# Kernel tuning notes

Hardware: AMD Instinct MI355X
Metric: run time of the kernel (lower is better)

The kernel has to match this reference:

```python
import jax, jax.numpy as jnp
import numpy as np

B, S, D, F, E = 4, 1024, 768, 3072, 8
TOP_K = 2


def setup_inputs() -> dict:
    key = jax.random.key(0)
    k0, k1, k2, k3 = jax.random.split(key, 4)
    x = jax.random.normal(k0, (B, S, D), dtype=jnp.float32)
    w_router = jax.random.normal(k1, (D, E), dtype=jnp.float32) * 0.02
    w1 = jax.random.normal(k2, (E, D, F), dtype=jnp.float32) * 0.02
    b1 = jnp.zeros((E, F), dtype=jnp.float32)
    w2 = jax.random.normal(k3, (E, F, D), dtype=jnp.float32) * 0.02
    b2 = jnp.zeros((E, D), dtype=jnp.float32)
    return {"x": x, "w_router": w_router, "w1": w1, "b1": b1, "w2": w2, "b2": b2}


def reference(x, w_router, w1, b1, w2, b2):
    # Router: logits [B,S,E] -> softmax -> top-k -> renormalize
    router_logits = jnp.einsum('bsd,de->bse', x, w_router)
    router_probs = jax.nn.softmax(router_logits, axis=-1)
    top_k_probs, top_k_idx = jax.lax.top_k(router_probs, TOP_K)  # [B,S,K]
    top_k_probs = top_k_probs / (jnp.sum(top_k_probs, axis=-1, keepdims=True) + 1e-8)
    # Combine weights [B,S,E]: weight for expert e if selected, else 0.
    # (top-k indices are distinct, so summing one-hots over k is exact.)
    combine = jnp.sum(
        jax.nn.one_hot(top_k_idx, E, dtype=x.dtype) * top_k_probs[..., None], axis=-2)
    # Dense per-expert FFN over ALL tokens (faithful to the original masked-dense math).
    h = jax.nn.gelu(jnp.einsum('bsd,edf->ebsf', x, w1) + b1[:, None, None, :],
                    approximate=False)  # [E,B,S,F]
    expert_out = jnp.einsum('ebsf,efd->ebsd', h, w2) + b2[:, None, None, :]  # [E,B,S,D]
    output = jnp.einsum('ebsd,bse->bsd', expert_out, combine)
    return output
```

## Files before the change

kernel.cpp:

```cpp
#include <hip/hip_runtime.h>
#include <math.h>

typedef __bf16 bf16x8 __attribute__((ext_vector_type(8)));
typedef float f32x4 __attribute__((ext_vector_type(4)));

#define B_ 4
#define S_ 1024
#define D_ 768
#define F_ 3072
#define E_ 8
#define NTOK 4096
#define NSLOTP 9216

__device__ __forceinline__ void gload_lds16(const void* g, void* s) {
  __builtin_amdgcn_global_load_lds((const __attribute__((address_space(1))) void*)g,
                                   (__attribute__((address_space(3))) void*)s, 16, 0, 0);
}

__device__ __forceinline__ float gelu_f(float v) {
  float u = v * (0.7978845608f + 0.0356774081f * v * v);
  float t = 1.f - 2.f / (1.f + __expf(2.f * u));
  return 0.5f * v * (1.f + t);
}

__global__ __launch_bounds__(256) void k_router(const float* __restrict__ x,
    const float* __restrict__ wr, int* __restrict__ tki, float* __restrict__ tkw) {
  int wid = threadIdx.x >> 6, lane = threadIdx.x & 63;
  int t = blockIdx.x * 4 + wid;
  const float* xp = x + (size_t)t * D_;
  float pa[E_];
#pragma unroll
  for (int e = 0; e < E_; ++e) pa[e] = 0.f;
#pragma unroll
  for (int it = 0; it < D_ / 64; ++it) {
    int d = it * 64 + lane;
    float xv = xp[d];
    const float4* wp = (const float4*)(wr + (size_t)d * E_);
    float4 a = wp[0], b = wp[1];
    pa[0] += xv * a.x; pa[1] += xv * a.y; pa[2] += xv * a.z; pa[3] += xv * a.w;
    pa[4] += xv * b.x; pa[5] += xv * b.y; pa[6] += xv * b.z; pa[7] += xv * b.w;
  }
#pragma unroll
  for (int e = 0; e < E_; ++e) {
    float v = pa[e];
    for (int off = 32; off; off >>= 1) v += __shfl_xor(v, off);
    pa[e] = v;
  }
  if (lane == 0) {
    float m = pa[0];
#pragma unroll
    for (int e = 1; e < E_; ++e) m = fmaxf(m, pa[e]);
    float p[E_], s = 0.f;
#pragma unroll
    for (int e = 0; e < E_; ++e) { p[e] = expf(pa[e] - m); s += p[e]; }
#pragma unroll
    for (int e = 0; e < E_; ++e) p[e] = p[e] / s;
    int i0 = 0; float b0 = p[0];
#pragma unroll
    for (int e = 1; e < E_; ++e) if (p[e] > b0) { b0 = p[e]; i0 = e; }
    int i1 = -1; float b1v = -1.f;
#pragma unroll
    for (int e = 0; e < E_; ++e) if (e != i0 && p[e] > b1v) { b1v = p[e]; i1 = e; }
    float den = b0 + b1v + 1e-8f;
    tki[t * 2] = i0; tki[t * 2 + 1] = i1;
    tkw[t * 2] = b0 / den; tkw[t * 2 + 1] = b1v / den;
  }
}

__global__ __launch_bounds__(256) void k_route_all(const int* __restrict__ tki,
    int* __restrict__ stok, int* __restrict__ tslot, int* __restrict__ aoff) {
  __shared__ int cl[256][E_];
  __shared__ int tot[E_];
  __shared__ int aoffA[E_ + 1];
  int tid = threadIdx.x;
  for (int i = tid; i < NSLOTP; i += 256) stok[i] = -1;
#pragma unroll
  for (int e = 0; e < E_; ++e) cl[tid][e] = 0;
  int t0 = tid * (NTOK / 256);
#pragma unroll
  for (int i = 0; i < NTOK / 256; ++i) {
    cl[tid][tki[(t0 + i) * 2]]++;
    cl[tid][tki[(t0 + i) * 2 + 1]]++;
  }
  __syncthreads();
  if (tid < E_) {
    int run = 0;
    for (int i = 0; i < 256; ++i) { int v = cl[i][tid]; cl[i][tid] = run; run += v; }
    tot[tid] = run;
  }
  __syncthreads();
  if (tid == 0) {
    int a = 0; aoffA[0] = 0; aoff[0] = 0;
    for (int e = 0; e < E_; ++e) { a += ((tot[e] + 127) >> 7) << 7; aoffA[e + 1] = a; aoff[e + 1] = a; }
  }
  __syncthreads();
#pragma unroll
  for (int i = 0; i < NTOK / 256; ++i) {
    int t = t0 + i;
#pragma unroll
    for (int k = 0; k < 2; ++k) {
      int e = tki[t * 2 + k];
      int pos = aoffA[e] + cl[tid][e];
      cl[tid][e]++;
      stok[pos] = t;
      tslot[t * 2 + k] = pos;
    }
  }
}

__global__ __launch_bounds__(256) void k_gather(const float* __restrict__ x,
    const int* __restrict__ stok, __bf16* __restrict__ Xg) {
  int i8 = blockIdx.x * 256 + threadIdx.x;
  int flat = i8 * 8;
  int row = flat / D_;
  int col = flat - row * D_;
  int tok = stok[row];
  bf16x8 v;
  if (tok >= 0) {
    const float4* s = (const float4*)(x + (size_t)tok * D_ + col);
    float4 a = s[0], b = s[1];
    v[0] = (__bf16)a.x; v[1] = (__bf16)a.y; v[2] = (__bf16)a.z; v[3] = (__bf16)a.w;
    v[4] = (__bf16)b.x; v[5] = (__bf16)b.y; v[6] = (__bf16)b.z; v[7] = (__bf16)b.w;
  } else {
#pragma unroll
    for (int k = 0; k < 8; ++k) v[k] = (__bf16)0.f;
  }
  *(bf16x8*)(Xg + (size_t)flat) = v;
}

__global__ __launch_bounds__(256) void k_transpose(const float* __restrict__ in,
    __bf16* __restrict__ outp, int R, int C) {
  __shared__ float Ts[64][65];
  int e = blockIdx.z;
  int r0 = blockIdx.y * 64, c0 = blockIdx.x * 64;
  const float* ip = in + (size_t)e * R * C;
  int lr = threadIdx.x >> 4;
  int lc = (threadIdx.x & 15) * 4;
#pragma unroll
  for (int it = 0; it < 4; ++it) {
    int r = lr + it * 16;
    float4 v = *(const float4*)(ip + (size_t)(r0 + r) * C + c0 + lc);
    Ts[r][lc] = v.x; Ts[r][lc + 1] = v.y; Ts[r][lc + 2] = v.z; Ts[r][lc + 3] = v.w;
  }
  __syncthreads();
  int rr = (threadIdx.x & 7) * 8;
  int cc = threadIdx.x >> 3;
  __bf16* op = outp + (size_t)e * R * C + r0 + rr;
#pragma unroll
  for (int it = 0; it < 2; ++it) {
    int c = cc + it * 32;
    bf16x8 v;
#pragma unroll
    for (int i = 0; i < 8; ++i) v[i] = (__bf16)Ts[rr + i][c];
    *(bf16x8*)(op + (size_t)(c0 + c) * R) = v;
  }
}

template<int KST, int N, int MODE, int KSPLIT>
__global__ __launch_bounds__(512, 4) void k_gemm(
    const __bf16* __restrict__ A, const __bf16* __restrict__ Bt,
    const float* __restrict__ bias, const int* __restrict__ aoff,
    __bf16* __restrict__ Hout, float* __restrict__ E0, float* __restrict__ E1) {
  constexpr int BN = 256;
  constexpr int ASZ = 128 * 32;
  constexpr int BSZ = BN * 32;
  constexpr int NK = KST / 32 / KSPLIT;
  constexpr int NB = N / BN;
  constexpr int NMB = NSLOTP / 128;
  constexpr int NWGB = NB * NMB;
  constexpr int NWG = NWGB * KSPLIT;

  __shared__ __align__(16) __bf16 Als[2 * ASZ];
  __shared__ __align__(16) __bf16 Bls[2 * BSZ];

  int bswz = (blockIdx.x & 7) * (NWG / 8) + (blockIdx.x >> 3);
  int kh = bswz / NWGB;
  int rem = bswz % NWGB;
  int mb = rem % NMB, nb = rem / NMB;
  int row0 = mb * 128;
  if (row0 >= aoff[E_]) return;
  int e = 0;
#pragma unroll
  for (int q = 0; q < E_; ++q) if (row0 >= aoff[q + 1]) e = q + 1;
  const __bf16* Bp = Bt + (size_t)e * D_ * F_;
  int kbase = kh * (KST / KSPLIT);

  int tid = threadIdx.x, w = tid >> 6, l = tid & 63;
  int lr = l >> 2, ls = l & 3;
  int fr = l & 15, fg = l >> 4;
  int wrow = (w >> 2) * 64, wcol = (w & 3) * 64;

  auto STAGE = [&](int kt, int b) {
    int k0 = kbase + kt * 32;
    {
      int rowA = w * 16 + lr;
      int sA = ls ^ ((rowA >> 1) & 3);
      gload_lds16(A + (size_t)(row0 + rowA) * KST + k0 + sA * 8, Als + b * ASZ + w * 512);
    }
#pragma unroll
    for (int q = 0; q < 2; ++q) {
      int idx = w * 2 + q;
      int rowB = idx * 16 + lr;
      int sB = ls ^ ((rowB >> 1) & 3);
      gload_lds16(Bp + (size_t)(nb * BN + rowB) * KST + k0 + sB * 8, Bls + b * BSZ + idx * 512);
    }
  };

  f32x4 acc[4][4] = {};
  STAGE(0, 0);
  asm volatile("s_waitcnt vmcnt(0)" ::: "memory");
  __builtin_amdgcn_sched_barrier(0);
  __builtin_amdgcn_s_barrier();
  for (int t = 0; t < NK; ++t) {
    int cur = t & 1;
    if (t + 1 < NK) STAGE(t + 1, cur ^ 1);
    __builtin_amdgcn_sched_barrier(0);
    bf16x8 af[4], bfr[4];
#pragma unroll
    for (int i = 0; i < 4; ++i) {
      int rl = wrow + i * 16 + fr;
      af[i] = *(const bf16x8*)(Als + cur * ASZ + rl * 32 + ((fg ^ ((rl >> 1) & 3)) << 3));
    }
#pragma unroll
    for (int j = 0; j < 4; ++j) {
      int nl = wcol + j * 16 + fr;
      bfr[j] = *(const bf16x8*)(Bls + cur * BSZ + nl * 32 + ((fg ^ ((nl >> 1) & 3)) << 3));
    }
#pragma unroll
    for (int i = 0; i < 4; ++i)
#pragma unroll
      for (int j = 0; j < 4; ++j)
        acc[i][j] = __builtin_amdgcn_mfma_f32_16x16x32_bf16(af[i], bfr[j], acc[i][j], 0, 0, 0);
    __builtin_amdgcn_sched_barrier(0);
    asm volatile("s_waitcnt vmcnt(0)" ::: "memory");
    __builtin_amdgcn_s_barrier();
  }

  if constexpr (MODE == 0) {
#pragma unroll
    for (int j = 0; j < 4; ++j) {
      int col = nb * BN + wcol + j * 16 + fr;
      float bv = bias[e * N + col];
#pragma unroll
      for (int i = 0; i < 4; ++i) {
#pragma unroll
        for (int r = 0; r < 4; ++r) {
          int row = row0 + wrow + i * 16 + fg * 4 + r;
          Hout[(size_t)row * N + col] = (__bf16)gelu_f(acc[i][j][r] + bv);
        }
      }
    }
  } else {
    float* Ep = (kh == 0) ? E0 : E1;
#pragma unroll
    for (int j = 0; j < 4; ++j) {
      int col = nb * BN + wcol + j * 16 + fr;
      float bv = (kh == 0) ? bias[e * N + col] : 0.f;
#pragma unroll
      for (int i = 0; i < 4; ++i) {
#pragma unroll
        for (int r = 0; r < 4; ++r) {
          int row = row0 + wrow + i * 16 + fg * 4 + r;
          Ep[(size_t)row * N + col] = acc[i][j][r] + bv;
        }
      }
    }
  }
}

__global__ __launch_bounds__(256) void k_combine(const float* __restrict__ E0,
    const float* __restrict__ E1, const int* __restrict__ tslot,
    const float* __restrict__ tkw, float* __restrict__ out) {
  int idx = blockIdx.x * 256 + threadIdx.x;
  int t = idx / (D_ / 4);
  int c4 = (idx - t * (D_ / 4)) * 4;
  int s0 = tslot[2 * t], s1 = tslot[2 * t + 1];
  float w0 = tkw[2 * t], w1 = tkw[2 * t + 1];
  float4 a = *(const float4*)(E0 + (size_t)s0 * D_ + c4);
  float4 b = *(const float4*)(E0 + (size_t)s1 * D_ + c4);
  float4 o;
  if (E1) {
    float4 a1 = *(const float4*)(E1 + (size_t)s0 * D_ + c4);
    float4 b1 = *(const float4*)(E1 + (size_t)s1 * D_ + c4);
    o.x = w0 * (a.x + a1.x) + w1 * (b.x + b1.x);
    o.y = w0 * (a.y + a1.y) + w1 * (b.y + b1.y);
    o.z = w0 * (a.z + a1.z) + w1 * (b.z + b1.z);
    o.w = w0 * (a.w + a1.w) + w1 * (b.w + b1.w);
  } else {
    o.x = w0 * a.x + w1 * b.x; o.y = w0 * a.y + w1 * b.y;
    o.z = w0 * a.z + w1 * b.z; o.w = w0 * a.w + w1 * b.w;
  }
  *(float4*)(out + (size_t)t * D_ + c4) = o;
}

extern "C" void kernel_launch(void* const* d_in, const int* in_sizes, int n_in,
                              void* d_out, int out_size, void* d_ws, size_t ws_size,
                              hipStream_t stream) {
  const float* x  = (const float*)d_in[0];
  const float* wr = (const float*)d_in[1];
  const float* w1 = (const float*)d_in[2];
  const float* b1 = (const float*)d_in[3];
  const float* w2 = (const float*)d_in[4];
  const float* b2 = (const float*)d_in[5];
  float* out = (float*)d_out;

  char* ws = (char*)d_ws;
  size_t o = 0;
  __bf16* w1t = (__bf16*)(ws + o); o += (size_t)E_ * D_ * F_ * 2;
  __bf16* Xg  = (__bf16*)(ws + o); o += (size_t)NSLOTP * D_ * 2;
  __bf16* w2t = (__bf16*)(ws + o); o += (size_t)E_ * D_ * F_ * 2;
  __bf16* H   = (__bf16*)(ws + o); o += (size_t)NSLOTP * F_ * 2;
  int*   tki  = (int*)(ws + o);   o += (size_t)NTOK * 2 * 4;
  float* tkw  = (float*)(ws + o); o += (size_t)NTOK * 2 * 4;
  int*   stok = (int*)(ws + o);   o += (size_t)NSLOTP * 4;
  int*   tslot= (int*)(ws + o);   o += (size_t)NTOK * 2 * 4;
  int*   aoff = (int*)(ws + o);   o += 64;
  float* E0   = (float*)w1t;
  float* E1   = (float*)(ws + o);
  size_t oE1  = o + (size_t)NSLOTP * D_ * 4;
  if (ws_size < o) return;
  bool split = (ws_size >= oE1);

  k_router<<<NTOK / 4, 256, 0, stream>>>(x, wr, tki, tkw);
  k_route_all<<<1, 256, 0, stream>>>(tki, stok, tslot, aoff);
  k_gather<<<(NSLOTP * D_ / 8) / 256, 256, 0, stream>>>(x, stok, Xg);
  k_transpose<<<dim3(F_ / 64, D_ / 64, E_), 256, 0, stream>>>(w1, w1t, D_, F_);
  k_transpose<<<dim3(D_ / 64, F_ / 64, E_), 256, 0, stream>>>(w2, w2t, F_, D_);
  k_gemm<D_, F_, 0, 1><<<(F_ / 256) * (NSLOTP / 128), 512, 0, stream>>>(
      Xg, w1t, b1, aoff, H, nullptr, nullptr);
  if (split) {
    k_gemm<F_, D_, 1, 2><<<2 * (D_ / 256) * (NSLOTP / 128), 512, 0, stream>>>(
        H, w2t, b2, aoff, nullptr, E0, E1);
    k_combine<<<NTOK * (D_ / 4) / 256, 256, 0, stream>>>(E0, E1, tslot, tkw, out);
  } else {
    k_gemm<F_, D_, 1, 1><<<(D_ / 256) * (NSLOTP / 128), 512, 0, stream>>>(
        H, w2t, b2, aoff, nullptr, E0, nullptr);
    k_combine<<<NTOK * (D_ / 4) / 256, 256, 0, stream>>>(E0, nullptr, tslot, tkw, out);
  }
}
```

Baseline: 212.9 us.

## Give first expert GEMM a dedicated triple-buffered K=64 pipeline with split MFMA phases

Splits the generic GEMM template into a specialised up-projection kernel and the existing down-projection kernel. The new up-projection kernel uses 64-wide K tiles with three LDS buffers, prefetching two stages ahead. Each iteration is split into two MFMA halves, with the next tile's global-to-LDS loads interleaved between them, explicit vmcnt/lgkmcnt waits, and raised wave priority around the MFMAs. This is meant to hide load latency and reduce barriers per FLOP, at the cost of much larger LDS use that drops occupancy to one workgroup per CU.

```diff
diff --git a/kernel.cpp b/kernel.cpp
--- a/kernel.cpp
+++ b/kernel.cpp
@@ -16,6 +16,15 @@
   __builtin_amdgcn_global_load_lds((const __attribute__((address_space(1))) void*)g,
                                    (__attribute__((address_space(3))) void*)s, 16, 0, 0);
 }
+
+template<int N> __device__ __forceinline__ void wait_vmcnt() {
+  if constexpr (N == 0)      asm volatile("s_waitcnt vmcnt(0)" ::: "memory");
+  else if constexpr (N == 6) asm volatile("s_waitcnt vmcnt(6)" ::: "memory");
+  else static_assert(N == 0, "unhandled vmcnt");
+}
+#define BAR()    asm volatile("s_barrier" ::: "memory")
+#define LGKM0()  do { asm volatile("s_waitcnt lgkmcnt(0)" ::: "memory"); \
+                      __builtin_amdgcn_sched_barrier(0); } while (0)
 
 __device__ __forceinline__ float gelu_f(float v) {
   float u = v * (0.7978845608f + 0.0356774081f * v * v);
@@ -156,11 +165,140 @@
   }
 }
 
-template<int KST, int N, int MODE, int KSPLIT>
-__global__ __launch_bounds__(512, 4) void k_gemm(
+__global__ __launch_bounds__(512, 1) void k_gemm1(
     const __bf16* __restrict__ A, const __bf16* __restrict__ Bt,
     const float* __restrict__ bias, const int* __restrict__ aoff,
-    __bf16* __restrict__ Hout, float* __restrict__ E0, float* __restrict__ E1) {
+    __bf16* __restrict__ Hout) {
+  constexpr int KST = D_;
+  constexpr int N = F_;
+  constexpr int NK = KST / 64;
+  constexpr int ASZ = 128 * 64;
+  constexpr int BSZ = 256 * 64;
+  constexpr int NB = N / 256, NMB = NSLOTP / 128, NWG = NB * NMB;
+
+  __shared__ __align__(16) __bf16 Als[3 * ASZ];
+  __shared__ __align__(16) __bf16 Bls[3 * BSZ];
+
+  int bswz = (blockIdx.x & 7) * (NWG / 8) + (blockIdx.x >> 3);
+  int mb = bswz % NMB, nb = bswz / NMB;
+  int row0 = mb * 128;
+  if (row0 >= aoff[E_]) return;
+  int e = 0;
+#pragma unroll
+  for (int q = 0; q < E_; ++q) if (row0 >= aoff[q + 1]) e = q + 1;
+  const __bf16* Bp = Bt + (size_t)e * D_ * F_;
+
+  int tid = threadIdx.x, w = tid >> 6, l = tid & 63;
+  int fr = l & 15, fg = l >> 4;
+  int wr = w >> 2, wc = w & 3;
+
+  int ur = tid >> 3;
+  int us = tid & 7;
+  int ukk = us >> 2, uf4 = us & 3;
+
+  auto SA = [&](int kt, int b) {
+#pragma unroll
+    for (int u = 0; u < 2; ++u) {
+      int r = u * 64 + ur;
+      int f4s = uf4 ^ ((r >> 1) & 3);
+      gload_lds16(A + (size_t)(row0 + r) * KST + kt * 64 + ukk * 32 + f4s * 8,
+                  Als + b * ASZ + u * 4096 + w * 512);
+    }
+  };
+  auto SB = [&](int kt, int b, int u0, int u1) {
+    for (int u = u0; u < u1; ++u) {
+      int r = u * 64 + ur;
+      int f4s = uf4 ^ ((r >> 1) & 3);
+      gload_lds16(Bp + (size_t)(nb * 256 + r) * KST + kt * 64 + ukk * 32 + f4s * 8,
+                  Bls + b * BSZ + u * 4096 + w * 512);
+    }
+  };
+
+  SA(0, 0); SB(0, 0, 0, 4);
+  SA(1, 1); SB(1, 1, 0, 4);
+
+  f32x4 acc[4][4] = {};
+  for (int t = 0; t < NK; ++t) {
+    int b = t % 3, bs = (t + 2) % 3;
+    bool st = (t + 2) < NK;
+    if (t + 1 < NK) wait_vmcnt<6>(); else wait_vmcnt<0>();
+    BAR();
+    __builtin_amdgcn_sched_barrier(0);
+    const __bf16* Ab = Als + b * ASZ;
+    const __bf16* Bb = Bls + b * BSZ;
+    bf16x8 af[4][2], bf0[2][2];
+#pragma unroll
+    for (int i = 0; i < 4; ++i) {
+      int r = wr * 64 + i * 16 + fr;
+      int sw = ((r >> 1) & 3);
+#pragma unroll
+      for (int kk = 0; kk < 2; ++kk)
+        af[i][kk] = *(const bf16x8*)(Ab + r * 64 + kk * 32 + ((fg ^ sw) << 3));
+    }
+#pragma unroll
+    for (int j = 0; j < 2; ++j) {
+      int n = wc * 64 + j * 16 + fr;
+      int sw = ((n >> 1) & 3);
+#pragma unroll
+      for (int kk = 0; kk < 2; ++kk)
+        bf0[j][kk] = *(const bf16x8*)(Bb + n * 64 + kk * 32 + ((fg ^ sw) << 3));
+    }
+    if (st) { SA(t + 2, bs); SB(t + 2, bs, 0, 2); }
+    LGKM0();
+    __builtin_amdgcn_s_setprio(1);
+#pragma unroll
+    for (int i = 0; i < 4; ++i)
+#pragma unroll
+      for (int j = 0; j < 2; ++j)
+#pragma unroll
+        for (int kk = 0; kk < 2; ++kk)
+          acc[i][j] = __builtin_amdgcn_mfma_f32_16x16x32_bf16(af[i][kk], bf0[j][kk], acc[i][j], 0, 0, 0);
+    __builtin_amdgcn_s_setprio(0);
+    __builtin_amdgcn_sched_barrier(0);
+    BAR();
+    bf16x8 bf1[2][2];
+#pragma unroll
+    for (int j = 0; j < 2; ++j) {
+      int n = wc * 64 + (2 + j) * 16 + fr;
+      int sw = ((n >> 1) & 3);
+#pragma unroll
+      for (int kk = 0; kk < 2; ++kk)
+        bf1[j][kk] = *(const bf16x8*)(Bb + n * 64 + kk * 32 + ((fg ^ sw) << 3));
+    }
+    if (st) SB(t + 2, bs, 2, 4);
+    LGKM0();
+    __builtin_amdgcn_s_setprio(1);
+#pragma unroll
+    for (int i = 0; i < 4; ++i)
+#pragma unroll
+      for (int j = 0; j < 2; ++j)
+#pragma unroll
+        for (int kk = 0; kk < 2; ++kk)
+          acc[i][2 + j] = __builtin_amdgcn_mfma_f32_16x16x32_bf16(af[i][kk], bf1[j][kk], acc[i][2 + j], 0, 0, 0);
+    __builtin_amdgcn_s_setprio(0);
+    __builtin_amdgcn_sched_barrier(0);
+  }
+
+#pragma unroll
+  for (int j = 0; j < 4; ++j) {
+    int col = nb * 256 + wc * 64 + j * 16 + fr;
+    float bv = bias[e * N + col];
+#pragma unroll
+    for (int i = 0; i < 4; ++i) {
+#pragma unroll
+      for (int r = 0; r < 4; ++r) {
+        int row = row0 + wr * 64 + i * 16 + fg * 4 + r;
+        Hout[(size_t)row * N + col] = (__bf16)gelu_f(acc[i][j][r] + bv);
+      }
+    }
+  }
+}
+
+template<int KST, int N, int KSPLIT>
+__global__ __launch_bounds__(512, 4) void k_gemm2(
+    const __bf16* __restrict__ A, const __bf16* __restrict__ Bt,
+    const float* __restrict__ bias, const int* __restrict__ aoff,
+    float* __restrict__ E0, float* __restrict__ E1) {
   constexpr int BN = 256;
   constexpr int ASZ = 128 * 32;
   constexpr int BSZ = BN * 32;
@@ -236,33 +374,17 @@
     __builtin_amdgcn_s_barrier();
   }
 
-  if constexpr (MODE == 0) {
-#pragma unroll
-    for (int j = 0; j < 4; ++j) {
-      int col = nb * BN + wcol + j * 16 + fr;
-      float bv = bias[e * N + col];
-#pragma unroll
-      for (int i = 0; i < 4; ++i) {
-#pragma unroll
-        for (int r = 0; r < 4; ++r) {
-          int row = row0 + wrow + i * 16 + fg * 4 + r;
-          Hout[(size_t)row * N + col] = (__bf16)gelu_f(acc[i][j][r] + bv);
-        }
-      }
-    }
-  } else {
-    float* Ep = (kh == 0) ? E0 : E1;
-#pragma unroll
-    for (int j = 0; j < 4; ++j) {
-      int col = nb * BN + wcol + j * 16 + fr;
-      float bv = (kh == 0) ? bias[e * N + col] : 0.f;
-#pragma unroll
-      for (int i = 0; i < 4; ++i) {
-#pragma unroll
-        for (int r = 0; r < 4; ++r) {
-          int row = row0 + wrow + i * 16 + fg * 4 + r;
-          Ep[(size_t)row * N + col] = acc[i][j][r] + bv;
-        }
+  float* Ep = (kh == 0) ? E0 : E1;
+#pragma unroll
+  for (int j = 0; j < 4; ++j) {
+    int col = nb * BN + wcol + j * 16 + fr;
+    float bv = (kh == 0) ? bias[e * N + col] : 0.f;
+#pragma unroll
+    for (int i = 0; i < 4; ++i) {
+#pragma unroll
+      for (int r = 0; r < 4; ++r) {
+        int row = row0 + wrow + i * 16 + fg * 4 + r;
+        Ep[(size_t)row * N + col] = acc[i][j][r] + bv;
       }
     }
   }
@@ -326,15 +448,14 @@
   k_gather<<<(NSLOTP * D_ / 8) / 256, 256, 0, stream>>>(x, stok, Xg);
   k_transpose<<<dim3(F_ / 64, D_ / 64, E_), 256, 0, stream>>>(w1, w1t, D_, F_);
   k_transpose<<<dim3(D_ / 64, F_ / 64, E_), 256, 0, stream>>>(w2, w2t, F_, D_);
-  k_gemm<D_, F_, 0, 1><<<(F_ / 256) * (NSLOTP / 128), 512, 0, stream>>>(
-      Xg, w1t, b1, aoff, H, nullptr, nullptr);
+  k_gemm1<<<(F_ / 256) * (NSLOTP / 128), 512, 0, stream>>>(Xg, w1t, b1, aoff, H);
   if (split) {
-    k_gemm<F_, D_, 1, 2><<<2 * (D_ / 256) * (NSLOTP / 128), 512, 0, stream>>>(
-        H, w2t, b2, aoff, nullptr, E0, E1);
+    k_gemm2<F_, D_, 2><<<2 * (D_ / 256) * (NSLOTP / 128), 512, 0, stream>>>(
+        H, w2t, b2, aoff, E0, E1);
     k_combine<<<NTOK * (D_ / 4) / 256, 256, 0, stream>>>(E0, E1, tslot, tkw, out);
   } else {
-    k_gemm<F_, D_, 1, 1><<<(D_ / 256) * (NSLOTP / 128), 512, 0, stream>>>(
-        H, w2t, b2, aoff, nullptr, E0, nullptr);
+    k_gemm2<F_, D_, 1><<<(D_ / 256) * (NSLOTP / 128), 512, 0, stream>>>(
+        H, w2t, b2, aoff, E0, nullptr);
     k_combine<<<NTOK * (D_ / 4) / 256, 256, 0, stream>>>(E0, nullptr, tslot, tkw, out);
   }
 }
```

Result: slower. 227.4 us (+6.8%).

## Store split-K partials in fp16 and reuse one transposed-weight buffer

Applied to the files above, without the earlier changes.

The second GEMM's split-K partial outputs are now written as fp16 instead of fp32, and the combine kernel reads 8 fp16 values per thread and accumulates in fp32. This halves partial-output traffic. The workspace is also reorganised so both weight transposes share a single buffer, with w2 transposed after GEMM1 finishes, so the split-K path is always taken. The risks are extra fp16 rounding on the partial sums and serialising the second transpose behind GEMM1.

```diff
diff --git a/kernel.cpp b/kernel.cpp
--- a/kernel.cpp
+++ b/kernel.cpp
@@ -3,6 +3,8 @@
 
 typedef __bf16 bf16x8 __attribute__((ext_vector_type(8)));
 typedef float f32x4 __attribute__((ext_vector_type(4)));
+typedef _Float16 f16;
+typedef _Float16 f16x8 __attribute__((ext_vector_type(8)));
 
 #define B_ 4
 #define S_ 1024
@@ -156,34 +158,30 @@
   }
 }
 
-template<int KST, int N, int MODE, int KSPLIT>
-__global__ __launch_bounds__(512, 4) void k_gemm(
+__global__ __launch_bounds__(512, 4) void k_gemm1(
     const __bf16* __restrict__ A, const __bf16* __restrict__ Bt,
     const float* __restrict__ bias, const int* __restrict__ aoff,
-    __bf16* __restrict__ Hout, float* __restrict__ E0, float* __restrict__ E1) {
+    __bf16* __restrict__ Hout) {
+  constexpr int KST = D_, N = F_;
   constexpr int BN = 256;
   constexpr int ASZ = 128 * 32;
   constexpr int BSZ = BN * 32;
-  constexpr int NK = KST / 32 / KSPLIT;
+  constexpr int NK = KST / 32;
   constexpr int NB = N / BN;
   constexpr int NMB = NSLOTP / 128;
-  constexpr int NWGB = NB * NMB;
-  constexpr int NWG = NWGB * KSPLIT;
+  constexpr int NWG = NB * NMB;
 
   __shared__ __align__(16) __bf16 Als[2 * ASZ];
   __shared__ __align__(16) __bf16 Bls[2 * BSZ];
 
   int bswz = (blockIdx.x & 7) * (NWG / 8) + (blockIdx.x >> 3);
-  int kh = bswz / NWGB;
-  int rem = bswz % NWGB;
-  int mb = rem % NMB, nb = rem / NMB;
+  int mb = bswz % NMB, nb = bswz / NMB;
   int row0 = mb * 128;
   if (row0 >= aoff[E_]) return;
   int e = 0;
 #pragma unroll
   for (int q = 0; q < E_; ++q) if (row0 >= aoff[q + 1]) e = q + 1;
   const __bf16* Bp = Bt + (size_t)e * D_ * F_;
-  int kbase = kh * (KST / KSPLIT);
 
   int tid = threadIdx.x, w = tid >> 6, l = tid & 63;
   int lr = l >> 2, ls = l & 3;
@@ -191,7 +189,7 @@
   int wrow = (w >> 2) * 64, wcol = (w & 3) * 64;
 
   auto STAGE = [&](int kt, int b) {
-    int k0 = kbase + kt * 32;
+    int k0 = kt * 32;
     {
       int rowA = w * 16 + lr;
       int sA = ls ^ ((rowA >> 1) & 3);
@@ -236,61 +234,135 @@
     __builtin_amdgcn_s_barrier();
   }
 
-  if constexpr (MODE == 0) {
+#pragma unroll
+  for (int j = 0; j < 4; ++j) {
+    int col = nb * BN + wcol + j * 16 + fr;
+    float bv = bias[e * N + col];
+#pragma unroll
+    for (int i = 0; i < 4; ++i) {
+#pragma unroll
+      for (int r = 0; r < 4; ++r) {
+        int row = row0 + wrow + i * 16 + fg * 4 + r;
+        Hout[(size_t)row * N + col] = (__bf16)gelu_f(acc[i][j][r] + bv);
+      }
+    }
+  }
+}
+
+__global__ __launch_bounds__(512, 4) void k_gemm2(
+    const __bf16* __restrict__ A, const __bf16* __restrict__ Bt,
+    const float* __restrict__ bias, const int* __restrict__ aoff,
+    f16* __restrict__ E0, f16* __restrict__ E1) {
+  constexpr int KST = F_, N = D_;
+  constexpr int BN = 256;
+  constexpr int ASZ = 128 * 32;
+  constexpr int BSZ = BN * 32;
+  constexpr int NK = KST / 32 / 2;
+  constexpr int NB = N / BN;
+  constexpr int NMB = NSLOTP / 128;
+  constexpr int NWGB = NB * NMB;
+  constexpr int NWG = NWGB * 2;
+
+  __shared__ __align__(16) __bf16 Als[2 * ASZ];
+  __shared__ __align__(16) __bf16 Bls[2 * BSZ];
+
+  int bswz = (blockIdx.x & 7) * (NWG / 8) + (blockIdx.x >> 3);
+  int kh = bswz / NWGB;
+  int rem = bswz % NWGB;
+  int mb = rem % NMB, nb = rem / NMB;
+  int row0 = mb * 128;
+  if (row0 >= aoff[E_]) return;
+  int e = 0;
+#pragma unroll
+  for (int q = 0; q < E_; ++q) if (row0 >= aoff[q + 1]) e = q + 1;
+  const __bf16* Bp = Bt + (size_t)e * D_ * F_;
+  int kbase = kh * (KST / 2);
+
+  int tid = threadIdx.x, w = tid >> 6, l = tid & 63;
+  int lr = l >> 2, ls = l & 3;
+  int fr = l & 15, fg = l >> 4;
+  int wrow = (w >> 2) * 64, wcol = (w & 3) * 64;
+
+  auto STAGE = [&](int kt, int b) {
+    int k0 = kbase + kt * 32;
+    {
+      int rowA = w * 16 + lr;
+      int sA = ls ^ ((rowA >> 1) & 3);
+      gload_lds16(A + (size_t)(row0 + rowA) * KST + k0 + sA * 8, Als + b * ASZ + w * 512);
+    }
+#pragma unroll
+    for (int q = 0; q < 2; ++q) {
+      int idx = w * 2 + q;
+      int rowB = idx * 16 + lr;
+      int sB = ls ^ ((rowB >> 1) & 3);
+      gload_lds16(Bp + (size_t)(nb * BN + rowB) * KST + k0 + sB * 8, Bls + b * BSZ + idx * 512);
+    }
+  };
+
+  f32x4 acc[4][4] = {};
+  STAGE(0, 0);
+  asm volatile("s_waitcnt vmcnt(0)" ::: "memory");
+  __builtin_amdgcn_sched_barrier(0);
+  __builtin_amdgcn_s_barrier();
+  for (int t = 0; t < NK; ++t) {
+    int cur = t & 1;
+    if (t + 1 < NK) STAGE(t + 1, cur ^ 1);
+    __builtin_amdgcn_sched_barrier(0);
+    bf16x8 af[4], bfr[4];
+#pragma unroll
+    for (int i = 0; i < 4; ++i) {
+      int rl = wrow + i * 16 + fr;
+      af[i] = *(const bf16x8*)(Als + cur * ASZ + rl * 32 + ((fg ^ ((rl >> 1) & 3)) << 3));
+    }
 #pragma unroll
     for (int j = 0; j < 4; ++j) {
-      int col = nb * BN + wcol + j * 16 + fr;
-      float bv = bias[e * N + col];
-#pragma unroll
-      for (int i = 0; i < 4; ++i) {
-#pragma unroll
-        for (int r = 0; r < 4; ++r) {
-          int row = row0 + wrow + i * 16 + fg * 4 + r;
-          Hout[(size_t)row * N + col] = (__bf16)gelu_f(acc[i][j][r] + bv);
-        }
+      int nl = wcol + j * 16 + fr;
+      bfr[j] = *(const bf16x8*)(Bls + cur * BSZ + nl * 32 + ((fg ^ ((nl >> 1) & 3)) << 3));
+    }
+#pragma unroll
+    for (int i = 0; i < 4; ++i)
+#pragma unroll
+      for (int j = 0; j < 4; ++j)
+        acc[i][j] = __builtin_amdgcn_mfma_f32_16x16x32_bf16(af[i], bfr[j], acc[i][j], 0, 0, 0);
+    __builtin_amdgcn_sched_barrier(0);
+    asm volatile("s_waitcnt vmcnt(0)" ::: "memory");
+    __builtin_amdgcn_s_barrier();
+  }
+
+  f16* Ep = (kh == 0) ? E0 : E1;
+#pragma unroll
+  for (int j = 0; j < 4; ++j) {
+    int col = nb * BN + wcol + j * 16 + fr;
+    float bv = (kh == 0) ? bias[e * N + col] : 0.f;
+#pragma unroll
+    for (int i = 0; i < 4; ++i) {
+#pragma unroll
+      for (int r = 0; r < 4; ++r) {
+        int row = row0 + wrow + i * 16 + fg * 4 + r;
+        Ep[(size_t)row * N + col] = (f16)(acc[i][j][r] + bv);
       }
     }
-  } else {
-    float* Ep = (kh == 0) ? E0 : E1;
-#pragma unroll
-    for (int j = 0; j < 4; ++j) {
-      int col = nb * BN + wcol + j * 16 + fr;
-      float bv = (kh == 0) ? bias[e * N + col] : 0.f;
-#pragma unroll
-      for (int i = 0; i < 4; ++i) {
-#pragma unroll
-        for (int r = 0; r < 4; ++r) {
-          int row = row0 + wrow + i * 16 + fg * 4 + r;
-          Ep[(size_t)row * N + col] = acc[i][j][r] + bv;
-        }
-      }
-    }
-  }
-}
-
-__global__ __launch_bounds__(256) void k_combine(const float* __restrict__ E0,
-    const float* __restrict__ E1, const int* __restrict__ tslot,
+  }
+}
+
+__global__ __launch_bounds__(256) void k_combine(const f16* __restrict__ E0,
+    const f16* __restrict__ E1, const int* __restrict__ tslot,
     const float* __restrict__ tkw, float* __restrict__ out) {
   int idx = blockIdx.x * 256 + threadIdx.x;
-  int t = idx / (D_ / 4);
-  int c4 = (idx - t * (D_ / 4)) * 4;
+  int t = idx / (D_ / 8);
+  int c8 = (idx - t * (D_ / 8)) * 8;
   int s0 = tslot[2 * t], s1 = tslot[2 * t + 1];
   float w0 = tkw[2 * t], w1 = tkw[2 * t + 1];
-  float4 a = *(const float4*)(E0 + (size_t)s0 * D_ + c4);
-  float4 b = *(const float4*)(E0 + (size_t)s1 * D_ + c4);
-  float4 o;
-  if (E1) {
-    float4 a1 = *(const float4*)(E1 + (size_t)s0 * D_ + c4);
-    float4 b1 = *(const float4*)(E1 + (size_t)s1 * D_ + c4);
-    o.x = w0 * (a.x + a1.x) + w1 * (b.x + b1.x);
-    o.y = w0 * (a.y + a1.y) + w1 * (b.y + b1.y);
-    o.z = w0 * (a.z + a1.z) + w1 * (b.z + b1.z);
-    o.w = w0 * (a.w + a1.w) + w1 * (b.w + b1.w);
-  } else {
-    o.x = w0 * a.x + w1 * b.x; o.y = w0 * a.y + w1 * b.y;
-    o.z = w0 * a.z + w1 * b.z; o.w = w0 * a.w + w1 * b.w;
-  }
-  *(float4*)(out + (size_t)t * D_ + c4) = o;
+  f16x8 a0 = *(const f16x8*)(E0 + (size_t)s0 * D_ + c8);
+  f16x8 b0 = *(const f16x8*)(E0 + (size_t)s1 * D_ + c8);
+  f16x8 a1 = *(const f16x8*)(E1 + (size_t)s0 * D_ + c8);
+  f16x8 b1 = *(const f16x8*)(E1 + (size_t)s1 * D_ + c8);
+  float o[8];
+#pragma unroll
+  for (int k = 0; k < 8; ++k)
+    o[k] = w0 * ((float)a0[k] + (float)a1[k]) + w1 * ((float)b0[k] + (float)b1[k]);
+  *(float4*)(out + (size_t)t * D_ + c8)     = *(float4*)&o[0];
+  *(float4*)(out + (size_t)t * D_ + c8 + 4) = *(float4*)&o[4];
 }
 
 extern "C" void kernel_launch(void* const* d_in, const int* in_sizes, int n_in,
@@ -306,35 +378,25 @@
 
   char* ws = (char*)d_ws;
   size_t o = 0;
-  __bf16* w1t = (__bf16*)(ws + o); o += (size_t)E_ * D_ * F_ * 2;
+  __bf16* wt  = (__bf16*)(ws + o); o += (size_t)E_ * D_ * F_ * 2;
   __bf16* Xg  = (__bf16*)(ws + o); o += (size_t)NSLOTP * D_ * 2;
-  __bf16* w2t = (__bf16*)(ws + o); o += (size_t)E_ * D_ * F_ * 2;
   __bf16* H   = (__bf16*)(ws + o); o += (size_t)NSLOTP * F_ * 2;
+  f16*   E1p  = (f16*)(ws + o);   o += (size_t)NSLOTP * D_ * 2;
   int*   tki  = (int*)(ws + o);   o += (size_t)NTOK * 2 * 4;
   float* tkw  = (float*)(ws + o); o += (size_t)NTOK * 2 * 4;
   int*   stok = (int*)(ws + o);   o += (size_t)NSLOTP * 4;
   int*   tslot= (int*)(ws + o);   o += (size_t)NTOK * 2 * 4;
   int*   aoff = (int*)(ws + o);   o += 64;
-  float* E0   = (float*)w1t;
-  float* E1   = (float*)(ws + o);
-  size_t oE1  = o + (size_t)NSLOTP * D_ * 4;
+  f16*   E0p  = (f16*)Xg;
   if (ws_size < o) return;
-  bool split = (ws_size >= oE1);
 
   k_router<<<NTOK / 4, 256, 0, stream>>>(x, wr, tki, tkw);
   k_route_all<<<1, 256, 0, stream>>>(tki, stok, tslot, aoff);
   k_gather<<<(NSLOTP * D_ / 8) / 256, 256, 0, stream>>>(x, stok, Xg);
-  k_transpose<<<dim3(F_ / 64, D_ / 64, E_), 256, 0, stream>>>(w1, w1t, D_, F_);
-  k_transpose<<<dim3(D_ / 64, F_ / 64, E_), 256, 0, stream>>>(w2, w2t, F_, D_);
-  k_gemm<D_, F_, 0, 1><<<(F_ / 256) * (NSLOTP / 128), 512, 0, stream>>>(
-      Xg, w1t, b1, aoff, H, nullptr, nullptr);
-  if (split) {
-    k_gemm<F_, D_, 1, 2><<<2 * (D_ / 256) * (NSLOTP / 128), 512, 0, stream>>>(
-        H, w2t, b2, aoff, nullptr, E0, E1);
-    k_combine<<<NTOK * (D_ / 4) / 256, 256, 0, stream>>>(E0, E1, tslot, tkw, out);
-  } else {
-    k_gemm<F_, D_, 1, 1><<<(D_ / 256) * (NSLOTP / 128), 512, 0, stream>>>(
-        H, w2t, b2, aoff, nullptr, E0, nullptr);
-    k_combine<<<NTOK * (D_ / 4) / 256, 256, 0, stream>>>(E0, nullptr, tslot, tkw, out);
-  }
-}
+  k_transpose<<<dim3(F_ / 64, D_ / 64, E_), 256, 0, stream>>>(w1, wt, D_, F_);
+  k_gemm1<<<(F_ / 256) * (NSLOTP / 128), 512, 0, stream>>>(Xg, wt, b1, aoff, H);
+  k_transpose<<<dim3(D_ / 64, F_ / 64, E_), 256, 0, stream>>>(w2, wt, F_, D_);
+  k_gemm2<<<2 * (D_ / 256) * (NSLOTP / 128), 512, 0, stream>>>(
+      H, wt, b2, aoff, E0p, E1p);
+  k_combine<<<NTOK * (D_ / 8) / 256, 256, 0, stream>>>(E0p, E1p, tslot, tkw, out);
+}
```

Result: faster. 202.1 us (-5.1%).
